# Optimization experiments

Measured on AMD Instinct MI355X. Metric: run time of the kernel, lower is better.

## Reference

```python
import jax, jax.numpy as jnp
import numpy as np
import math

B, Z, D = 1024, 32768, 128

def setup_inputs() -> dict:
    key = jax.random.key(0)
    k1, k2, k3 = jax.random.split(key, 3)
    z_sparse = jax.random.randint(k1, (B, Z), 0, 2, dtype=jnp.int32)
    context_embedding = jax.random.normal(k2, (B, D), dtype=jnp.float32)
    embd_table = jax.random.normal(k3, (Z, D), dtype=jnp.float32)  # nn.Embedding weight
    return {"z_sparse": z_sparse, "context_embedding": context_embedding, "embd_table": embd_table}

def reference(z_sparse, context_embedding, embd_table):
    # mask[b, z] = feature z active in batch b  (matches (z_sparse > 0).nonzero())
    mask = z_sparse > 0  # [B, Z]
    # attn_scores = (ctx * emb).sum(-1) / sqrt(D), densified over all (b, z)
    scores = (context_embedding @ embd_table.T) / math.sqrt(embd_table.shape[1])  # [B, Z]
    # per-batch softmax over active features only
    masked = jnp.where(mask, scores, -jnp.inf)
    w = jax.nn.softmax(masked, axis=-1)
    w = jnp.where(mask, w, 0.0)  # zero inactive (also kills NaN for all-empty rows)
    # scatter-add of emb * weight == weighted matmul against the table
    out = w @ embd_table  # [B, D]
    counts = jnp.clip(jnp.sum(mask, axis=-1), 1, None)  # bincount(...).clamp(min=1)
    return out / counts[:, None].astype(out.dtype)
```

## Files before the change

### kernel.cpp

```cpp
#include <hip/hip_runtime.h>
#include <stdint.h>

#define B_SZ 1024
#define Z_SZ 32768
#define D_SZ 128
#define NZ   32
#define CZ   (Z_SZ / NZ)
#define TZ   64
#define ITERS (CZ / TZ)
#define TBLK 64
#define WROWS 16

#define SEMB_STRIDE  136
#define SEMBT_STRIDE 72
#define SP_STRIDE    72
#define ST_STRIDE    136

#define NB_TAB  (Z_SZ / 64)

#define WS_O   0
#define WS_M   (NZ * B_SZ * D_SZ)
#define WS_L   (WS_M + NZ * B_SZ)
#define WS_C   (WS_L + NZ * B_SZ)
#define WS_TAB (WS_C + NZ * B_SZ)

typedef short bf16x8 __attribute__((ext_vector_type(8)));
typedef float f32x4  __attribute__((ext_vector_type(4)));

#if __has_builtin(__builtin_amdgcn_exp2f)
#define EXP2F(x) __builtin_amdgcn_exp2f(x)
#else
#define EXP2F(x) exp2f(x)
#endif

__device__ __forceinline__ unsigned short f2bf(float f) {
    union { float f; uint32_t u; } v; v.f = f;
    uint32_t u = v.u;
    u = (u + 0x7FFFu + ((u >> 16) & 1u)) >> 16;
    return (unsigned short)u;
}

__global__ __launch_bounds__(256) void prep(
    const float*    __restrict__ emb,
    unsigned short* __restrict__ embR,
    unsigned short* __restrict__ embT)
{
    __shared__ __align__(16) unsigned short st[64 * ST_STRIDE];
    const int z0 = blockIdx.x * 64;
    const int t  = threadIdx.x;
    {
        const int r = t >> 2, q = t & 3;
        const float* src = emb + (size_t)(z0 + r) * D_SZ + q * 32;
        unsigned short* dR = embR + (size_t)(z0 + r) * D_SZ + q * 32;
        unsigned short* dL = st + r * ST_STRIDE + q * 32;
#pragma unroll
        for (int u = 0; u < 8; ++u) {
            float4 x = *(const float4*)(src + 4 * u);
            ushort4 h;
            h.x = f2bf(x.x); h.y = f2bf(x.y); h.z = f2bf(x.z); h.w = f2bf(x.w);
            *(ushort4*)(dR + 4 * u) = h;
            *(ushort4*)(dL + 4 * u) = h;
        }
    }
    __syncthreads();
    {
        const int lane = t & 63, w = t >> 6;
#pragma unroll
        for (int i = 0; i < 4; ++i) {
            const int d = w * 32 + i * 8 + (lane >> 3);
            const int c = lane & 7;
            bf16x8 v;
#pragma unroll
            for (int k = 0; k < 8; ++k) v[k] = (short)st[(c * 8 + k) * ST_STRIDE + d];
            *(bf16x8*)(embT + (size_t)d * Z_SZ + z0 + c * 8) = v;
        }
    }
}

__global__ __launch_bounds__(256, 2) void attn_part(
    const int*            __restrict__ zs,
    const float*          __restrict__ ctx,
    const unsigned short* __restrict__ embR,
    const unsigned short* __restrict__ embT,
    float*                __restrict__ ws)
{
    __shared__ __align__(16) unsigned short s_emb [TZ   * SEMB_STRIDE];
    __shared__ __align__(16) unsigned short s_embT[D_SZ * SEMBT_STRIDE];
    __shared__ __align__(16) unsigned short s_P   [4 * WROWS * SP_STRIDE];

    const int tid  = threadIdx.x;
    const int wave = tid >> 6;
    const int lane = tid & 63;
    const int l15  = lane & 15;
    const int quad = lane >> 4;

    const int bg     = blockIdx.x;
    const int ch     = blockIdx.y;
    const int z_base = ch * CZ;
    const int wb0    = bg * TBLK + wave * WROWS;
    const int brow   = wb0 + l15;

    const int srow = tid >> 2, sq3 = tid & 3;
    const int sd   = tid >> 1, sh  = tid & 1;

    const int* zrow = zs + (size_t)brow * Z_SZ + quad * 4;

    bf16x8 afrag[4];
    {
        const float scale = (float)(1.4426950408889634 * 0.08838834764831845);
        const float* crow = ctx + (size_t)brow * D_SZ;
#pragma unroll
        for (int ks = 0; ks < 4; ++ks) {
            const float* p = crow + ks * 32 + quad * 8;
            float4 x0 = *(const float4*)(p);
            float4 x1 = *(const float4*)(p + 4);
            bf16x8 a;
            a[0] = (short)f2bf(x0.x * scale); a[1] = (short)f2bf(x0.y * scale);
            a[2] = (short)f2bf(x0.z * scale); a[3] = (short)f2bf(x0.w * scale);
            a[4] = (short)f2bf(x1.x * scale); a[5] = (short)f2bf(x1.y * scale);
            a[6] = (short)f2bf(x1.z * scale); a[7] = (short)f2bf(x1.w * scale);
            afrag[ks] = a;
        }
    }

    float m_s = -1e30f, l_s = 0.f;
    int   cnt = 0;
    f32x4 acc2[8];
#pragma unroll
    for (int n = 0; n < 8; ++n) { acc2[n][0]=0.f; acc2[n][1]=0.f; acc2[n][2]=0.f; acc2[n][3]=0.f; }

    bf16x8 rA[4], rT[4];
    int4   mc[4], mn[4];
    {
        const unsigned short* srcR = embR + (size_t)(z_base + srow) * D_SZ + sq3 * 32;
        const unsigned short* srcT = embT + (size_t)sd * Z_SZ + z_base + sh * 32;
#pragma unroll
        for (int u = 0; u < 4; ++u) {
            rA[u] = *(const bf16x8*)(srcR + u * 8);
            rT[u] = *(const bf16x8*)(srcT + u * 8);
        }
#pragma unroll
        for (int nt = 0; nt < 4; ++nt) mc[nt] = *(const int4*)(zrow + z_base + nt * 16);
    }

    for (int it = 0; it < ITERS; ++it) {
        __syncthreads();

        {
            unsigned short* dst = s_emb + srow * SEMB_STRIDE + sq3 * 32;
#pragma unroll
            for (int u = 0; u < 4; ++u) *(bf16x8*)(dst + u * 8) = rA[u];
        }
        {
            unsigned short* dst = s_embT + sd * SEMBT_STRIDE + sh * 32;
#pragma unroll
            for (int u = 0; u < 4; ++u) *(bf16x8*)(dst + u * 8) = rT[u];
        }

        __syncthreads();

        if (it + 1 < ITERS) {
            const int z0n = z_base + (it + 1) * TZ;
            const unsigned short* srcR = embR + (size_t)(z0n + srow) * D_SZ + sq3 * 32;
            const unsigned short* srcT = embT + (size_t)sd * Z_SZ + z0n + sh * 32;
#pragma unroll
            for (int u = 0; u < 4; ++u) {
                rA[u] = *(const bf16x8*)(srcR + u * 8);
                rT[u] = *(const bf16x8*)(srcT + u * 8);
            }
#pragma unroll
            for (int nt = 0; nt < 4; ++nt) mn[nt] = *(const int4*)(zrow + z0n + nt * 16);
        }

        f32x4 sfr[4];
#pragma unroll
        for (int nt = 0; nt < 4; ++nt) {
            f32x4 c; c[0]=0.f; c[1]=0.f; c[2]=0.f; c[3]=0.f;
            const unsigned short* bb = s_emb + (nt * 16 + l15) * SEMB_STRIDE + quad * 8;
#pragma unroll
            for (int ks = 0; ks < 4; ++ks) {
                bf16x8 ef = *(const bf16x8*)(bb + ks * 32);
                c = __builtin_amdgcn_mfma_f32_16x16x32_bf16(ef, afrag[ks], c, 0, 0, 0);
            }
            sfr[nt] = c;
        }

        int bit[4][4];
#pragma unroll
        for (int nt = 0; nt < 4; ++nt) {
            bit[nt][0] = (mc[nt].x > 0) ? 1 : 0;
            bit[nt][1] = (mc[nt].y > 0) ? 1 : 0;
            bit[nt][2] = (mc[nt].z > 0) ? 1 : 0;
            bit[nt][3] = (mc[nt].w > 0) ? 1 : 0;
            cnt += bit[nt][0] + bit[nt][1] + bit[nt][2] + bit[nt][3];
        }

        float tm = -1e30f;
#pragma unroll
        for (int nt = 0; nt < 4; ++nt) {
            float a0 = bit[nt][0] ? sfr[nt][0] : -1e30f;
            float a1 = bit[nt][1] ? sfr[nt][1] : -1e30f;
            float a2 = bit[nt][2] ? sfr[nt][2] : -1e30f;
            float a3 = bit[nt][3] ? sfr[nt][3] : -1e30f;
            tm = fmaxf(tm, fmaxf(fmaxf(a0, a1), fmaxf(a2, a3)));
        }
        tm = fmaxf(tm, __shfl_xor(tm, 16));
        tm = fmaxf(tm, __shfl_xor(tm, 32));

        if (__any(tm > m_s + 8.f)) {
            float mnew = fmaxf(m_s, tm);
            float al = EXP2F(m_s - mnew);
            m_s = mnew;
            l_s *= al;
#pragma unroll
            for (int n = 0; n < 8; ++n) acc2[n] *= al;
        }

        unsigned short* pwv = s_P + wave * (WROWS * SP_STRIDE) + l15 * SP_STRIDE + quad * 4;
        float ps = 0.f;
#pragma unroll
        for (int nt = 0; nt < 4; ++nt) {
            float p0 = bit[nt][0] ? EXP2F(sfr[nt][0] - m_s) : 0.f;
            float p1 = bit[nt][1] ? EXP2F(sfr[nt][1] - m_s) : 0.f;
            float p2 = bit[nt][2] ? EXP2F(sfr[nt][2] - m_s) : 0.f;
            float p3 = bit[nt][3] ? EXP2F(sfr[nt][3] - m_s) : 0.f;
            ps += (p0 + p1) + (p2 + p3);
            ushort4 h;
            h.x = f2bf(p0); h.y = f2bf(p1); h.z = f2bf(p2); h.w = f2bf(p3);
            *(ushort4*)(pwv + nt * 16) = h;
        }
        ps += __shfl_xor(ps, 16);
        ps += __shfl_xor(ps, 32);
        l_s += ps;

        const unsigned short* pb = s_P + wave * (WROWS * SP_STRIDE) + l15 * SP_STRIDE + quad * 8;
        bf16x8 pA0 = *(const bf16x8*)(pb);
        bf16x8 pA1 = *(const bf16x8*)(pb + 32);
#pragma unroll
        for (int nt2 = 0; nt2 < 8; ++nt2) {
            const unsigned short* tb = s_embT + (nt2 * 16 + l15) * SEMBT_STRIDE + quad * 8;
            bf16x8 e0 = *(const bf16x8*)(tb);
            bf16x8 e1 = *(const bf16x8*)(tb + 32);
            acc2[nt2] = __builtin_amdgcn_mfma_f32_16x16x32_bf16(e0, pA0, acc2[nt2], 0, 0, 0);
            acc2[nt2] = __builtin_amdgcn_mfma_f32_16x16x32_bf16(e1, pA1, acc2[nt2], 0, 0, 0);
        }

#pragma unroll
        for (int nt = 0; nt < 4; ++nt) mc[nt] = mn[nt];
    }

    {
        float* orow = ws + WS_O + ((size_t)ch * B_SZ + brow) * D_SZ;
#pragma unroll
        for (int nt2 = 0; nt2 < 8; ++nt2) {
            *(f32x4*)(orow + nt2 * 16 + quad * 4) = acc2[nt2];
        }
    }
    cnt += __shfl_xor(cnt, 16);
    cnt += __shfl_xor(cnt, 32);
    if (lane < 16) {
        ws[WS_M + ch * B_SZ + brow] = m_s;
        ws[WS_L + ch * B_SZ + brow] = l_s;
        ws[WS_C + ch * B_SZ + brow] = (float)cnt;
    }
}

__global__ __launch_bounds__(128) void attn_reduce(
    const float* __restrict__ ws, float* __restrict__ out)
{
    const int b = blockIdx.x;
    const int d = threadIdx.x;
    const float* mP = ws + WS_M;
    const float* lP = ws + WS_L;
    const float* cP = ws + WS_C;

    float M = -1e30f;
#pragma unroll
    for (int c = 0; c < NZ; ++c) M = fmaxf(M, mP[c * B_SZ + b]);

    float L = 0.f, C = 0.f, acc = 0.f;
#pragma unroll
    for (int c = 0; c < NZ; ++c) {
        float w = EXP2F(mP[c * B_SZ + b] - M);
        L += lP[c * B_SZ + b] * w;
        C += cP[c * B_SZ + b];
        acc += ws[WS_O + ((size_t)c * B_SZ + b) * D_SZ + d] * w;
    }
    float cntv = fmaxf(C, 1.0f);
    out[(size_t)b * D_SZ + d] = (L > 0.f) ? acc / (L * cntv) : 0.f;
}

extern "C" void kernel_launch(void* const* d_in, const int* in_sizes, int n_in,
                              void* d_out, int out_size, void* d_ws, size_t ws_size,
                              hipStream_t stream) {
    (void)in_sizes; (void)n_in; (void)out_size; (void)ws_size;
    const int*   zs  = (const int*)  d_in[0];
    const float* ctx = (const float*)d_in[1];
    const float* emb = (const float*)d_in[2];
    float* out = (float*)d_out;
    float* ws  = (float*)d_ws;

    unsigned short* embR = (unsigned short*)(ws + WS_TAB);
    unsigned short* embT = embR + (size_t)Z_SZ * D_SZ;

    prep<<<NB_TAB, 256, 0, stream>>>(emb, embR, embT);

    dim3 grid1(B_SZ / TBLK, NZ);
    attn_part<<<grid1, 256, 0, stream>>>(zs, ctx, embR, embT, ws);
    attn_reduce<<<B_SZ, 128, 0, stream>>>(ws, out);
}
```

Measured before the change: 240.6 us.

## Read embedding tiles directly from global memory instead of staging in LDS

Removes the shared-memory staging of the row-major and transposed embedding tiles, along with the register prefetch double-buffer and both block barriers per iteration. Each wave now loads its MFMA operand fragments straight from global memory, relying on L1/L2 caching since the four waves of a block read the same tile. The Z split doubles to 64 chunks and launch bounds rise to 4 blocks per SU to recover latency hiding through occupancy. The cost is redundant global/cache traffic across waves, unhidden load latency without explicit prefetch, and twice as many partial results for the combine step.

```diff
diff --git a/kernel.cpp b/kernel.cpp
--- a/kernel.cpp
+++ b/kernel.cpp
@@ -4,15 +4,13 @@
 #define B_SZ 1024
 #define Z_SZ 32768
 #define D_SZ 128
-#define NZ   32
+#define NZ   64
 #define CZ   (Z_SZ / NZ)
 #define TZ   64
 #define ITERS (CZ / TZ)
 #define TBLK 64
 #define WROWS 16
 
-#define SEMB_STRIDE  136
-#define SEMBT_STRIDE 72
 #define SP_STRIDE    72
 #define ST_STRIDE    136
 
@@ -77,16 +75,14 @@
     }
 }
 
-__global__ __launch_bounds__(256, 2) void attn_part(
+__global__ __launch_bounds__(256, 4) void attn_part(
     const int*            __restrict__ zs,
     const float*          __restrict__ ctx,
     const unsigned short* __restrict__ embR,
     const unsigned short* __restrict__ embT,
     float*                __restrict__ ws)
 {
-    __shared__ __align__(16) unsigned short s_emb [TZ   * SEMB_STRIDE];
-    __shared__ __align__(16) unsigned short s_embT[D_SZ * SEMBT_STRIDE];
-    __shared__ __align__(16) unsigned short s_P   [4 * WROWS * SP_STRIDE];
+    __shared__ __align__(16) unsigned short s_P[4 * WROWS * SP_STRIDE];
 
     const int tid  = threadIdx.x;
     const int wave = tid >> 6;
@@ -99,9 +95,6 @@
     const int z_base = ch * CZ;
     const int wb0    = bg * TBLK + wave * WROWS;
     const int brow   = wb0 + l15;
-
-    const int srow = tid >> 2, sq3 = tid & 3;
-    const int sd   = tid >> 1, sh  = tid & 1;
 
     const int* zrow = zs + (size_t)brow * Z_SZ + quad * 4;
 
@@ -129,57 +122,21 @@
 #pragma unroll
     for (int n = 0; n < 8; ++n) { acc2[n][0]=0.f; acc2[n][1]=0.f; acc2[n][2]=0.f; acc2[n][3]=0.f; }
 
-    bf16x8 rA[4], rT[4];
-    int4   mc[4], mn[4];
-    {
-        const unsigned short* srcR = embR + (size_t)(z_base + srow) * D_SZ + sq3 * 32;
-        const unsigned short* srcT = embT + (size_t)sd * Z_SZ + z_base + sh * 32;
-#pragma unroll
-        for (int u = 0; u < 4; ++u) {
-            rA[u] = *(const bf16x8*)(srcR + u * 8);
-            rT[u] = *(const bf16x8*)(srcT + u * 8);
-        }
-#pragma unroll
-        for (int nt = 0; nt < 4; ++nt) mc[nt] = *(const int4*)(zrow + z_base + nt * 16);
-    }
-
     for (int it = 0; it < ITERS; ++it) {
-        __syncthreads();
-
-        {
-            unsigned short* dst = s_emb + srow * SEMB_STRIDE + sq3 * 32;
-#pragma unroll
-            for (int u = 0; u < 4; ++u) *(bf16x8*)(dst + u * 8) = rA[u];
-        }
-        {
-            unsigned short* dst = s_embT + sd * SEMBT_STRIDE + sh * 32;
-#pragma unroll
-            for (int u = 0; u < 4; ++u) *(bf16x8*)(dst + u * 8) = rT[u];
-        }
-
-        __syncthreads();
-
-        if (it + 1 < ITERS) {
-            const int z0n = z_base + (it + 1) * TZ;
-            const unsigned short* srcR = embR + (size_t)(z0n + srow) * D_SZ + sq3 * 32;
-            const unsigned short* srcT = embT + (size_t)sd * Z_SZ + z0n + sh * 32;
-#pragma unroll
-            for (int u = 0; u < 4; ++u) {
-                rA[u] = *(const bf16x8*)(srcR + u * 8);
-                rT[u] = *(const bf16x8*)(srcT + u * 8);
-            }
-#pragma unroll
-            for (int nt = 0; nt < 4; ++nt) mn[nt] = *(const int4*)(zrow + z0n + nt * 16);
-        }
+        const int z0 = z_base + it * TZ;
+
+        int4 mc[4];
+#pragma unroll
+        for (int nt = 0; nt < 4; ++nt) mc[nt] = *(const int4*)(zrow + z0 + nt * 16);
 
         f32x4 sfr[4];
 #pragma unroll
         for (int nt = 0; nt < 4; ++nt) {
             f32x4 c; c[0]=0.f; c[1]=0.f; c[2]=0.f; c[3]=0.f;
-            const unsigned short* bb = s_emb + (nt * 16 + l15) * SEMB_STRIDE + quad * 8;
+            const unsigned short* er = embR + (size_t)(z0 + nt * 16 + l15) * D_SZ + quad * 8;
 #pragma unroll
             for (int ks = 0; ks < 4; ++ks) {
-                bf16x8 ef = *(const bf16x8*)(bb + ks * 32);
+                bf16x8 ef = *(const bf16x8*)(er + ks * 32);
                 c = __builtin_amdgcn_mfma_f32_16x16x32_bf16(ef, afrag[ks], c, 0, 0, 0);
             }
             sfr[nt] = c;
@@ -238,15 +195,12 @@
         bf16x8 pA1 = *(const bf16x8*)(pb + 32);
 #pragma unroll
         for (int nt2 = 0; nt2 < 8; ++nt2) {
-            const unsigned short* tb = s_embT + (nt2 * 16 + l15) * SEMBT_STRIDE + quad * 8;
-            bf16x8 e0 = *(const bf16x8*)(tb);
-            bf16x8 e1 = *(const bf16x8*)(tb + 32);
+            const unsigned short* te = embT + (size_t)(nt2 * 16 + l15) * Z_SZ + z0 + quad * 8;
+            bf16x8 e0 = *(const bf16x8*)(te);
+            bf16x8 e1 = *(const bf16x8*)(te + 32);
             acc2[nt2] = __builtin_amdgcn_mfma_f32_16x16x32_bf16(e0, pA0, acc2[nt2], 0, 0, 0);
             acc2[nt2] = __builtin_amdgcn_mfma_f32_16x16x32_bf16(e1, pA1, acc2[nt2], 0, 0, 0);
         }
-
-#pragma unroll
-        for (int nt = 0; nt < 4; ++nt) mc[nt] = mn[nt];
     }
 
     {
```

After: 313.8 us. 1.3x slower.

## Switch attention partial kernel to 32x32x16 MFMA with 128-row batch tiles

Applied to the files above, without the earlier changes.

Replaces the 16x16x32 bf16 MFMA tiles with 32x32x16 ones, so each wave now handles 32 batch rows and the block covers 128 rows. It also doubles the Z split to 64 chunks and drops the register prefetch of the embedding tiles, loading them straight into shared memory each iteration. The larger tiles halve how often each embedding tile is re-read across batch blocks and use the bigger MFMA shape. In exchange the kernel needs more accumulator registers, loses load/compute overlap for the embedding tiles, and writes a workspace twice as large for the reduce step.

```diff
diff --git a/kernel.cpp b/kernel.cpp
--- a/kernel.cpp
+++ b/kernel.cpp
@@ -4,12 +4,13 @@
 #define B_SZ 1024
 #define Z_SZ 32768
 #define D_SZ 128
-#define NZ   32
+#define NZ   64
 #define CZ   (Z_SZ / NZ)
 #define TZ   64
 #define ITERS (CZ / TZ)
-#define TBLK 64
-#define WROWS 16
+#define TBLK 128
+#define NWAVE 4
+#define WROWS 32
 
 #define SEMB_STRIDE  136
 #define SEMBT_STRIDE 72
@@ -24,8 +25,9 @@
 #define WS_C   (WS_L + NZ * B_SZ)
 #define WS_TAB (WS_C + NZ * B_SZ)
 
-typedef short bf16x8 __attribute__((ext_vector_type(8)));
-typedef float f32x4  __attribute__((ext_vector_type(4)));
+typedef short bf16x8  __attribute__((ext_vector_type(8)));
+typedef float f32x4   __attribute__((ext_vector_type(4)));
+typedef float f32x16  __attribute__((ext_vector_type(16)));
 
 #if __has_builtin(__builtin_amdgcn_exp2f)
 #define EXP2F(x) __builtin_amdgcn_exp2f(x)
@@ -86,32 +88,32 @@
 {
     __shared__ __align__(16) unsigned short s_emb [TZ   * SEMB_STRIDE];
     __shared__ __align__(16) unsigned short s_embT[D_SZ * SEMBT_STRIDE];
-    __shared__ __align__(16) unsigned short s_P   [4 * WROWS * SP_STRIDE];
+    __shared__ __align__(16) unsigned short s_P   [NWAVE * WROWS * SP_STRIDE];
 
     const int tid  = threadIdx.x;
     const int wave = tid >> 6;
     const int lane = tid & 63;
-    const int l15  = lane & 15;
-    const int quad = lane >> 4;
+    const int l31  = lane & 31;
+    const int hi   = lane >> 5;
 
     const int bg     = blockIdx.x;
     const int ch     = blockIdx.y;
     const int z_base = ch * CZ;
     const int wb0    = bg * TBLK + wave * WROWS;
-    const int brow   = wb0 + l15;
+    const int brow   = wb0 + l31;
 
     const int srow = tid >> 2, sq3 = tid & 3;
     const int sd   = tid >> 1, sh  = tid & 1;
 
-    const int* zrow = zs + (size_t)brow * Z_SZ + quad * 4;
-
-    bf16x8 afrag[4];
+    const int* zrow = zs + (size_t)brow * Z_SZ + hi * 4;
+
+    bf16x8 afrag[8];
     {
         const float scale = (float)(1.4426950408889634 * 0.08838834764831845);
         const float* crow = ctx + (size_t)brow * D_SZ;
 #pragma unroll
-        for (int ks = 0; ks < 4; ++ks) {
-            const float* p = crow + ks * 32 + quad * 8;
+        for (int ks = 0; ks < 8; ++ks) {
+            const float* p = crow + ks * 16 + hi * 8;
             float4 x0 = *(const float4*)(p);
             float4 x1 = *(const float4*)(p + 4);
             bf16x8 a;
@@ -125,86 +127,92 @@
 
     float m_s = -1e30f, l_s = 0.f;
     int   cnt = 0;
-    f32x4 acc2[8];
-#pragma unroll
-    for (int n = 0; n < 8; ++n) { acc2[n][0]=0.f; acc2[n][1]=0.f; acc2[n][2]=0.f; acc2[n][3]=0.f; }
-
-    bf16x8 rA[4], rT[4];
-    int4   mc[4], mn[4];
-    {
-        const unsigned short* srcR = embR + (size_t)(z_base + srow) * D_SZ + sq3 * 32;
-        const unsigned short* srcT = embT + (size_t)sd * Z_SZ + z_base + sh * 32;
-#pragma unroll
-        for (int u = 0; u < 4; ++u) {
-            rA[u] = *(const bf16x8*)(srcR + u * 8);
-            rT[u] = *(const bf16x8*)(srcT + u * 8);
-        }
-#pragma unroll
-        for (int nt = 0; nt < 4; ++nt) mc[nt] = *(const int4*)(zrow + z_base + nt * 16);
-    }
+    f32x16 acc[4];
+#pragma unroll
+    for (int n = 0; n < 4; ++n) {
+#pragma unroll
+        for (int e = 0; e < 16; ++e) acc[n][e] = 0.f;
+    }
+
+    int4 mc[2][4], mn[2][4];
+#pragma unroll
+    for (int nt = 0; nt < 2; ++nt)
+#pragma unroll
+        for (int g = 0; g < 4; ++g)
+            mc[nt][g] = *(const int4*)(zrow + z_base + nt * 32 + g * 8);
 
     for (int it = 0; it < ITERS; ++it) {
+        const int z0 = z_base + it * TZ;
         __syncthreads();
 
         {
+            const unsigned short* srcR = embR + (size_t)(z0 + srow) * D_SZ + sq3 * 32;
             unsigned short* dst = s_emb + srow * SEMB_STRIDE + sq3 * 32;
-#pragma unroll
-            for (int u = 0; u < 4; ++u) *(bf16x8*)(dst + u * 8) = rA[u];
+            bf16x8 v0 = *(const bf16x8*)(srcR);      bf16x8 v1 = *(const bf16x8*)(srcR + 8);
+            bf16x8 v2 = *(const bf16x8*)(srcR + 16); bf16x8 v3 = *(const bf16x8*)(srcR + 24);
+            *(bf16x8*)(dst)      = v0; *(bf16x8*)(dst + 8)  = v1;
+            *(bf16x8*)(dst + 16) = v2; *(bf16x8*)(dst + 24) = v3;
         }
         {
+            const unsigned short* srcT = embT + (size_t)sd * Z_SZ + z0 + sh * 32;
             unsigned short* dst = s_embT + sd * SEMBT_STRIDE + sh * 32;
-#pragma unroll
-            for (int u = 0; u < 4; ++u) *(bf16x8*)(dst + u * 8) = rT[u];
+            bf16x8 v0 = *(const bf16x8*)(srcT);      bf16x8 v1 = *(const bf16x8*)(srcT + 8);
+            bf16x8 v2 = *(const bf16x8*)(srcT + 16); bf16x8 v3 = *(const bf16x8*)(srcT + 24);
+            *(bf16x8*)(dst)      = v0; *(bf16x8*)(dst + 8)  = v1;
+            *(bf16x8*)(dst + 16) = v2; *(bf16x8*)(dst + 24) = v3;
         }
 
         __syncthreads();
 
         if (it + 1 < ITERS) {
-            const int z0n = z_base + (it + 1) * TZ;
-            const unsigned short* srcR = embR + (size_t)(z0n + srow) * D_SZ + sq3 * 32;
-            const unsigned short* srcT = embT + (size_t)sd * Z_SZ + z0n + sh * 32;
-#pragma unroll
-            for (int u = 0; u < 4; ++u) {
-                rA[u] = *(const bf16x8*)(srcR + u * 8);
-                rT[u] = *(const bf16x8*)(srcT + u * 8);
-            }
-#pragma unroll
-            for (int nt = 0; nt < 4; ++nt) mn[nt] = *(const int4*)(zrow + z0n + nt * 16);
-        }
-
-        f32x4 sfr[4];
-#pragma unroll
-        for (int nt = 0; nt < 4; ++nt) {
-            f32x4 c; c[0]=0.f; c[1]=0.f; c[2]=0.f; c[3]=0.f;
-            const unsigned short* bb = s_emb + (nt * 16 + l15) * SEMB_STRIDE + quad * 8;
-#pragma unroll
-            for (int ks = 0; ks < 4; ++ks) {
-                bf16x8 ef = *(const bf16x8*)(bb + ks * 32);
-                c = __builtin_amdgcn_mfma_f32_16x16x32_bf16(ef, afrag[ks], c, 0, 0, 0);
+            const int z0n = z0 + TZ;
+#pragma unroll
+            for (int nt = 0; nt < 2; ++nt)
+#pragma unroll
+                for (int g = 0; g < 4; ++g)
+                    mn[nt][g] = *(const int4*)(zrow + z0n + nt * 32 + g * 8);
+        }
+
+        f32x16 sfr[2];
+#pragma unroll
+        for (int nt = 0; nt < 2; ++nt) {
+            f32x16 c;
+#pragma unroll
+            for (int e = 0; e < 16; ++e) c[e] = 0.f;
+            const unsigned short* bb = s_emb + (nt * 32 + l31) * SEMB_STRIDE + hi * 8;
+#pragma unroll
+            for (int ks = 0; ks < 8; ++ks) {
+                bf16x8 ef = *(const bf16x8*)(bb + ks * 16);
+                c = __builtin_amdgcn_mfma_f32_32x32x16_bf16(ef, afrag[ks], c, 0, 0, 0);
             }
             sfr[nt] = c;
         }
 
-        int bit[4][4];
-#pragma unroll
-        for (int nt = 0; nt < 4; ++nt) {
-            bit[nt][0] = (mc[nt].x > 0) ? 1 : 0;
-            bit[nt][1] = (mc[nt].y > 0) ? 1 : 0;
-            bit[nt][2] = (mc[nt].z > 0) ? 1 : 0;
-            bit[nt][3] = (mc[nt].w > 0) ? 1 : 0;
-            cnt += bit[nt][0] + bit[nt][1] + bit[nt][2] + bit[nt][3];
+        int bit[2][16];
+#pragma unroll
+        for (int nt = 0; nt < 2; ++nt) {
+#pragma unroll
+            for (int g = 0; g < 4; ++g) {
+                bit[nt][4*g+0] = (mc[nt][g].x > 0) ? 1 : 0;
+                bit[nt][4*g+1] = (mc[nt][g].y > 0) ? 1 : 0;
+                bit[nt][4*g+2] = (mc[nt][g].z > 0) ? 1 : 0;
+                bit[nt][4*g+3] = (mc[nt][g].w > 0) ? 1 : 0;
+                cnt += bit[nt][4*g+0] + bit[nt][4*g+1] + bit[nt][4*g+2] + bit[nt][4*g+3];
+            }
         }
 
         float tm = -1e30f;
 #pragma unroll
-        for (int nt = 0; nt < 4; ++nt) {
-            float a0 = bit[nt][0] ? sfr[nt][0] : -1e30f;
-            float a1 = bit[nt][1] ? sfr[nt][1] : -1e30f;
-            float a2 = bit[nt][2] ? sfr[nt][2] : -1e30f;
-            float a3 = bit[nt][3] ? sfr[nt][3] : -1e30f;
-            tm = fmaxf(tm, fmaxf(fmaxf(a0, a1), fmaxf(a2, a3)));
-        }
-        tm = fmaxf(tm, __shfl_xor(tm, 16));
+        for (int nt = 0; nt < 2; ++nt) {
+#pragma unroll
+            for (int r = 0; r < 16; r += 4) {
+                float a0 = bit[nt][r+0] ? sfr[nt][r+0] : -1e30f;
+                float a1 = bit[nt][r+1] ? sfr[nt][r+1] : -1e30f;
+                float a2 = bit[nt][r+2] ? sfr[nt][r+2] : -1e30f;
+                float a3 = bit[nt][r+3] ? sfr[nt][r+3] : -1e30f;
+                tm = fmaxf(tm, fmaxf(fmaxf(a0, a1), fmaxf(a2, a3)));
+            }
+        }
         tm = fmaxf(tm, __shfl_xor(tm, 32));
 
         if (__any(tm > m_s + 8.f)) {
@@ -213,52 +221,65 @@
             m_s = mnew;
             l_s *= al;
 #pragma unroll
-            for (int n = 0; n < 8; ++n) acc2[n] *= al;
-        }
-
-        unsigned short* pwv = s_P + wave * (WROWS * SP_STRIDE) + l15 * SP_STRIDE + quad * 4;
+            for (int n = 0; n < 4; ++n)
+#pragma unroll
+                for (int e = 0; e < 16; ++e) acc[n][e] *= al;
+        }
+
+        unsigned short* pwv = s_P + wave * (WROWS * SP_STRIDE) + l31 * SP_STRIDE + hi * 4;
         float ps = 0.f;
 #pragma unroll
-        for (int nt = 0; nt < 4; ++nt) {
-            float p0 = bit[nt][0] ? EXP2F(sfr[nt][0] - m_s) : 0.f;
-            float p1 = bit[nt][1] ? EXP2F(sfr[nt][1] - m_s) : 0.f;
-            float p2 = bit[nt][2] ? EXP2F(sfr[nt][2] - m_s) : 0.f;
-            float p3 = bit[nt][3] ? EXP2F(sfr[nt][3] - m_s) : 0.f;
-            ps += (p0 + p1) + (p2 + p3);
-            ushort4 h;
-            h.x = f2bf(p0); h.y = f2bf(p1); h.z = f2bf(p2); h.w = f2bf(p3);
-            *(ushort4*)(pwv + nt * 16) = h;
-        }
-        ps += __shfl_xor(ps, 16);
+        for (int nt = 0; nt < 2; ++nt) {
+#pragma unroll
+            for (int g = 0; g < 4; ++g) {
+                float p0 = bit[nt][4*g+0] ? EXP2F(sfr[nt][4*g+0] - m_s) : 0.f;
+                float p1 = bit[nt][4*g+1] ? EXP2F(sfr[nt][4*g+1] - m_s) : 0.f;
+                float p2 = bit[nt][4*g+2] ? EXP2F(sfr[nt][4*g+2] - m_s) : 0.f;
+                float p3 = bit[nt][4*g+3] ? EXP2F(sfr[nt][4*g+3] - m_s) : 0.f;
+                ps += (p0 + p1) + (p2 + p3);
+                ushort4 h;
+                h.x = f2bf(p0); h.y = f2bf(p1); h.z = f2bf(p2); h.w = f2bf(p3);
+                *(ushort4*)(pwv + nt * 32 + g * 8) = h;
+            }
+        }
         ps += __shfl_xor(ps, 32);
         l_s += ps;
 
-        const unsigned short* pb = s_P + wave * (WROWS * SP_STRIDE) + l15 * SP_STRIDE + quad * 8;
-        bf16x8 pA0 = *(const bf16x8*)(pb);
-        bf16x8 pA1 = *(const bf16x8*)(pb + 32);
-#pragma unroll
-        for (int nt2 = 0; nt2 < 8; ++nt2) {
-            const unsigned short* tb = s_embT + (nt2 * 16 + l15) * SEMBT_STRIDE + quad * 8;
-            bf16x8 e0 = *(const bf16x8*)(tb);
-            bf16x8 e1 = *(const bf16x8*)(tb + 32);
-            acc2[nt2] = __builtin_amdgcn_mfma_f32_16x16x32_bf16(e0, pA0, acc2[nt2], 0, 0, 0);
-            acc2[nt2] = __builtin_amdgcn_mfma_f32_16x16x32_bf16(e1, pA1, acc2[nt2], 0, 0, 0);
-        }
-
-#pragma unroll
-        for (int nt = 0; nt < 4; ++nt) mc[nt] = mn[nt];
+        const unsigned short* pb = s_P + wave * (WROWS * SP_STRIDE) + l31 * SP_STRIDE + hi * 8;
+        bf16x8 pfrag[4];
+#pragma unroll
+        for (int ks2 = 0; ks2 < 4; ++ks2) pfrag[ks2] = *(const bf16x8*)(pb + ks2 * 16);
+#pragma unroll
+        for (int nt2 = 0; nt2 < 4; ++nt2) {
+            const unsigned short* tb = s_embT + (nt2 * 32 + l31) * SEMBT_STRIDE + hi * 8;
+#pragma unroll
+            for (int ks2 = 0; ks2 < 4; ++ks2) {
+                bf16x8 ta = *(const bf16x8*)(tb + ks2 * 16);
+                acc[nt2] = __builtin_amdgcn_mfma_f32_32x32x16_bf16(ta, pfrag[ks2], acc[nt2], 0, 0, 0);
+            }
+        }
+
+#pragma unroll
+        for (int nt = 0; nt < 2; ++nt)
+#pragma unroll
+            for (int g = 0; g < 4; ++g) mc[nt][g] = mn[nt][g];
     }
 
     {
         float* orow = ws + WS_O + ((size_t)ch * B_SZ + brow) * D_SZ;
 #pragma unroll
-        for (int nt2 = 0; nt2 < 8; ++nt2) {
-            *(f32x4*)(orow + nt2 * 16 + quad * 4) = acc2[nt2];
-        }
-    }
-    cnt += __shfl_xor(cnt, 16);
+        for (int nt2 = 0; nt2 < 4; ++nt2) {
+#pragma unroll
+            for (int g = 0; g < 4; ++g) {
+                f32x4 v;
+                v[0] = acc[nt2][4*g+0]; v[1] = acc[nt2][4*g+1];
+                v[2] = acc[nt2][4*g+2]; v[3] = acc[nt2][4*g+3];
+                *(f32x4*)(orow + nt2 * 32 + g * 8 + hi * 4) = v;
+            }
+        }
+    }
     cnt += __shfl_xor(cnt, 32);
-    if (lane < 16) {
+    if (lane < 32) {
         ws[WS_M + ch * B_SZ + brow] = m_s;
         ws[WS_L + ch * B_SZ + brow] = l_s;
         ws[WS_C + ch * B_SZ + brow] = (float)cnt;
```

Result: no change. 239.7 us (-0.4%).
